# Optimization experiments

Hardware: AMD Instinct MI355X
Metric: run time of the kernel (lower is better)

## Reference

```python
import jax, jax.numpy as jnp
import numpy as np

N_NODES = 50000
N_EDGES = 800000
HIDDEN = 128
N_GRAPHS = 64


def _linear_init(key, fan_in, shape):
    # torch.nn.Linear default init: U(-1/sqrt(fan_in), 1/sqrt(fan_in))
    bound = 1.0 / np.sqrt(fan_in)
    return jax.random.uniform(key, shape, jnp.float32, -bound, bound)


def setup_inputs() -> dict:
    key = jax.random.key(0)
    ks = jax.random.split(key, 13)
    x = jax.random.normal(ks[0], (N_NODES, HIDDEN), jnp.float32)
    edge_index = jax.random.randint(ks[1], (2, N_EDGES), 0, N_NODES, dtype=jnp.int64)
    batch = jnp.sort(jax.random.randint(ks[2], (N_NODES,), 0, N_GRAPHS, dtype=jnp.int64))
    H = HIDDEN
    return {
        "x": x,
        "edge_index": edge_index,
        "batch": batch,
        "W1a": _linear_init(ks[3], H, (H, H)),
        "b1a": _linear_init(ks[4], H, (H,)),
        "W2a": _linear_init(ks[5], H, (H, H)),
        "b2a": _linear_init(ks[6], H, (H,)),
        "W1b": _linear_init(ks[7], H, (H, H)),
        "b1b": _linear_init(ks[8], H, (H,)),
        "W2b": _linear_init(ks[9], H, (H, H)),
        "b2b": _linear_init(ks[10], H, (H,)),
        "Wfc": _linear_init(ks[11], H, (H, 1)),
        "bfc": _linear_init(ks[12], H, (1,)),
    }


def _gin_conv(x, src, dst, W1, b1, W2, b2):
    # GINConv with eps=0: mlp((1+eps)*x + sum_{j->i} x_j)
    agg = jax.ops.segment_sum(x[src], dst, num_segments=N_NODES) + x
    h = jax.nn.gelu(agg @ W1 + b1, approximate=False)  # exact erf GELU (torch default)
    return jax.nn.gelu(h @ W2 + b2, approximate=False)


def reference(x, edge_index, batch, W1a, b1a, W2a, b2a, W1b, b1b, W2b, b2b, Wfc, bfc):
    src, dst = edge_index[0], edge_index[1]  # messages flow src -> dst (PyG convention)
    h = _gin_conv(x, src, dst, W1a, b1a, W2a, b2a)
    h = _gin_conv(h, src, dst, W1b, b1b, W2b, b2b)
    y = h @ Wfc + bfc  # [N, 1]
    return jax.ops.segment_sum(y, batch, num_segments=N_GRAPHS)  # [G, 1]
```

## Files before the change

kernel.cpp:

```cpp
#include <hip/hip_runtime.h>
#include <hip/hip_bf16.h>
#include <math.h>

#define N_NODES 50000
#define N_EDGES 800000
#define HID 128
#define N_GRAPHS 64
#define BCAP 64

typedef __bf16 bfv8 __attribute__((ext_vector_type(8)));
typedef float f32x4 __attribute__((ext_vector_type(4)));

__device__ __forceinline__ unsigned short f2bf(float f) {
    unsigned int u = __float_as_uint(f);
    u += 0x7fff + ((u >> 16) & 1);
    return (unsigned short)(u >> 16);
}
__device__ __forceinline__ float bflo(unsigned int u) { return __uint_as_float(u << 16); }
__device__ __forceinline__ float bfhi(unsigned int u) { return __uint_as_float(u & 0xffff0000u); }

__device__ __forceinline__ float gelu_f(float x) {
    float x3 = x * x * x;
    float z = 1.5957691216f * x + 0.0713548162f * x3;
    float e = __expf(z);
    float t = 1.f - 2.f / (e + 1.f);
    return 0.5f * x * (1.f + t);
}

__global__ void conv_bf16(const float4* __restrict__ in, ushort4* __restrict__ out, int n4) {
    for (int i = blockIdx.x * blockDim.x + threadIdx.x; i < n4; i += gridDim.x * blockDim.x) {
        float4 v = in[i];
        ushort4 o;
        o.x = f2bf(v.x); o.y = f2bf(v.y); o.z = f2bf(v.z); o.w = f2bf(v.w);
        out[i] = o;
    }
}

__global__ void prep_weights(const float* __restrict__ W1a, const float* __restrict__ W2a,
                             const float* __restrict__ W1b, const float* __restrict__ W2b,
                             unsigned short* __restrict__ out) {
    int i = blockIdx.x * blockDim.x + threadIdx.x;
    if (i >= 4 * HID * HID) return;
    int m = i >> 14;
    int r = (i >> 7) & 127;
    int c = i & 127;
    const float* W = (m == 0) ? W1a : (m == 1) ? W2a : (m == 2) ? W1b : W2b;
    out[i] = f2bf(W[c * HID + r]);
}

__global__ void bucket_insert(const int* __restrict__ src, const int* __restrict__ dst,
                              int* __restrict__ counts, unsigned short* __restrict__ bucket) {
    int e = blockIdx.x * blockDim.x + threadIdx.x;
    if (e < N_EDGES) {
        int d = dst[e];
        int pos = atomicAdd(&counts[d], 1);
        if (pos < BCAP) bucket[(size_t)d * BCAP + pos] = (unsigned short)src[e];
    }
}

__global__ __launch_bounds__(256) void aggregate8(const unsigned short* __restrict__ xb,
                                                  const int* __restrict__ counts,
                                                  const unsigned short* __restrict__ bucket,
                                                  unsigned short* __restrict__ agg) {
    int node = blockIdx.x * 4 + (threadIdx.x >> 6);
    if (node >= N_NODES) return;
    int lane = threadIdx.x & 63;
    int g = lane >> 3;
    int c = lane & 7;
    int cnt = min(counts[node], BCAP);
    int eidx = (int)bucket[(size_t)node * BCAP + lane];
    float a[16];
    #pragma unroll
    for (int j = 0; j < 16; ++j) a[j] = 0.f;
    int kmax = (cnt + 7) >> 3;
    #pragma unroll 2
    for (int k = 0; k < kmax; ++k) {
        int i = 8 * k + g;
        int s = __shfl(eidx, (i < cnt) ? i : 0);
        if (i < cnt) {
            const unsigned short* row = xb + (size_t)s * HID + c * 16;
            uint4 u0 = *(const uint4*)(row);
            uint4 u1 = *(const uint4*)(row + 8);
            a[0] += bflo(u0.x); a[1] += bfhi(u0.x);
            a[2] += bflo(u0.y); a[3] += bfhi(u0.y);
            a[4] += bflo(u0.z); a[5] += bfhi(u0.z);
            a[6] += bflo(u0.w); a[7] += bfhi(u0.w);
            a[8] += bflo(u1.x); a[9] += bfhi(u1.x);
            a[10] += bflo(u1.y); a[11] += bfhi(u1.y);
            a[12] += bflo(u1.z); a[13] += bfhi(u1.z);
            a[14] += bflo(u1.w); a[15] += bfhi(u1.w);
        }
    }
    #pragma unroll
    for (int j = 0; j < 16; ++j) {
        a[j] += __shfl_xor(a[j], 8);
        a[j] += __shfl_xor(a[j], 16);
        a[j] += __shfl_xor(a[j], 32);
    }
    if (g == 0) {
        const unsigned short* row = xb + (size_t)node * HID + c * 16;
        uint4 u0 = *(const uint4*)(row);
        uint4 u1 = *(const uint4*)(row + 8);
        a[0] += bflo(u0.x); a[1] += bfhi(u0.x);
        a[2] += bflo(u0.y); a[3] += bfhi(u0.y);
        a[4] += bflo(u0.z); a[5] += bfhi(u0.z);
        a[6] += bflo(u0.w); a[7] += bfhi(u0.w);
        a[8] += bflo(u1.x); a[9] += bfhi(u1.x);
        a[10] += bflo(u1.y); a[11] += bfhi(u1.y);
        a[12] += bflo(u1.z); a[13] += bfhi(u1.z);
        a[14] += bflo(u1.w); a[15] += bfhi(u1.w);
        uint4 o0, o1;
        o0.x = (unsigned int)f2bf(a[0]) | ((unsigned int)f2bf(a[1]) << 16);
        o0.y = (unsigned int)f2bf(a[2]) | ((unsigned int)f2bf(a[3]) << 16);
        o0.z = (unsigned int)f2bf(a[4]) | ((unsigned int)f2bf(a[5]) << 16);
        o0.w = (unsigned int)f2bf(a[6]) | ((unsigned int)f2bf(a[7]) << 16);
        o1.x = (unsigned int)f2bf(a[8]) | ((unsigned int)f2bf(a[9]) << 16);
        o1.y = (unsigned int)f2bf(a[10]) | ((unsigned int)f2bf(a[11]) << 16);
        o1.z = (unsigned int)f2bf(a[12]) | ((unsigned int)f2bf(a[13]) << 16);
        o1.w = (unsigned int)f2bf(a[14]) | ((unsigned int)f2bf(a[15]) << 16);
        unsigned short* orow = agg + (size_t)node * HID + c * 16;
        *(uint4*)(orow) = o0;
        *(uint4*)(orow + 8) = o1;
    }
}

#define LDP 136
__global__ __launch_bounds__(512) void mlp_fused(const unsigned short* __restrict__ A,
                                                 const unsigned short* __restrict__ Wt1,
                                                 const float* __restrict__ b1,
                                                 const unsigned short* __restrict__ Wt2,
                                                 const float* __restrict__ b2,
                                                 unsigned short* __restrict__ out, int nrows) {
    __shared__ __align__(16) unsigned short sA[128][LDP];
    __shared__ __align__(16) unsigned short sT[128][LDP];
    const int t = threadIdx.x;
    const int row0 = blockIdx.x * 128;

    #pragma unroll
    for (int rr = 0; rr < 4; ++rr) {
        int idx = t + rr * 512;
        int r = idx >> 4;
        int cb = (idx & 15) * 8;
        int gr = row0 + r;
        ulonglong2 v = {0ull, 0ull};
        if (gr < nrows) v = *(const ulonglong2*)(A + (size_t)gr * HID + cb);
        *(ulonglong2*)(&sA[r][cb]) = v;
    }

    const int w = t >> 6;
    const int l = t & 63;
    const int lr = l & 15;
    const int lkg = l >> 4;
    const int lk = lkg * 8;
    const int cw = w * 16 + lr;

    bfv8 w1f[4], w2f[4];
    #pragma unroll
    for (int kc = 0; kc < 4; ++kc) {
        w1f[kc] = *(const bfv8*)(Wt1 + (size_t)cw * HID + kc * 32 + lk);
        w2f[kc] = *(const bfv8*)(Wt2 + (size_t)cw * HID + kc * 32 + lk);
    }
    float bias1 = b1[cw];
    float bias2 = b2[cw];
    __syncthreads();

    f32x4 acc[8];
    #pragma unroll
    for (int m = 0; m < 8; ++m) acc[m] = (f32x4){0.f, 0.f, 0.f, 0.f};
    #pragma unroll
    for (int m = 0; m < 8; ++m) {
        #pragma unroll
        for (int kc = 0; kc < 4; ++kc) {
            bfv8 af = *(const bfv8*)(&sA[m * 16 + lr][kc * 32 + lk]);
            acc[m] = __builtin_amdgcn_mfma_f32_16x16x32_bf16(af, w1f[kc], acc[m], 0, 0, 0);
        }
    }
    #pragma unroll
    for (int m = 0; m < 8; ++m) {
        #pragma unroll
        for (int i = 0; i < 4; ++i) {
            float v = gelu_f(acc[m][i] + bias1);
            sT[m * 16 + lkg * 4 + i][cw] = f2bf(v);
        }
    }
    __syncthreads();

    #pragma unroll
    for (int m = 0; m < 8; ++m) acc[m] = (f32x4){0.f, 0.f, 0.f, 0.f};
    #pragma unroll
    for (int m = 0; m < 8; ++m) {
        #pragma unroll
        for (int kc = 0; kc < 4; ++kc) {
            bfv8 af = *(const bfv8*)(&sT[m * 16 + lr][kc * 32 + lk]);
            acc[m] = __builtin_amdgcn_mfma_f32_16x16x32_bf16(af, w2f[kc], acc[m], 0, 0, 0);
        }
    }
    #pragma unroll
    for (int m = 0; m < 8; ++m) {
        #pragma unroll
        for (int i = 0; i < 4; ++i) {
            float v = gelu_f(acc[m][i] + bias2);
            sA[m * 16 + lkg * 4 + i][cw] = f2bf(v);
        }
    }
    __syncthreads();
    #pragma unroll
    for (int rr = 0; rr < 4; ++rr) {
        int idx = t + rr * 512;
        int r = idx >> 4;
        int cb = (idx & 15) * 8;
        int gr = row0 + r;
        if (gr < nrows)
            *(ulonglong2*)(out + (size_t)gr * HID + cb) = *(const ulonglong2*)(&sA[r][cb]);
    }
}

__global__ __launch_bounds__(512) void mlp_final(const unsigned short* __restrict__ A,
                                                 const unsigned short* __restrict__ Wt1,
                                                 const float* __restrict__ b1,
                                                 const unsigned short* __restrict__ Wt2,
                                                 const float* __restrict__ b2,
                                                 const float* __restrict__ Wfc,
                                                 const float* __restrict__ bfc,
                                                 const int* __restrict__ batch,
                                                 float* __restrict__ out, int nrows) {
    __shared__ __align__(16) unsigned short sA[128][LDP];
    __shared__ __align__(16) unsigned short sT[128][LDP];
    __shared__ float bins[N_GRAPHS];
    const int t = threadIdx.x;
    const int row0 = blockIdx.x * 128;
    if (t < N_GRAPHS) bins[t] = 0.f;

    #pragma unroll
    for (int rr = 0; rr < 4; ++rr) {
        int idx = t + rr * 512;
        int r = idx >> 4;
        int cb = (idx & 15) * 8;
        int gr = row0 + r;
        ulonglong2 v = {0ull, 0ull};
        if (gr < nrows) v = *(const ulonglong2*)(A + (size_t)gr * HID + cb);
        *(ulonglong2*)(&sA[r][cb]) = v;
    }

    const int w = t >> 6;
    const int l = t & 63;
    const int lr = l & 15;
    const int lkg = l >> 4;
    const int lk = lkg * 8;
    const int cw = w * 16 + lr;

    bfv8 w1f[4], w2f[4];
    #pragma unroll
    for (int kc = 0; kc < 4; ++kc) {
        w1f[kc] = *(const bfv8*)(Wt1 + (size_t)cw * HID + kc * 32 + lk);
        w2f[kc] = *(const bfv8*)(Wt2 + (size_t)cw * HID + kc * 32 + lk);
    }
    float bias1 = b1[cw];
    float bias2 = b2[cw];
    __syncthreads();

    f32x4 acc[8];
    #pragma unroll
    for (int m = 0; m < 8; ++m) acc[m] = (f32x4){0.f, 0.f, 0.f, 0.f};
    #pragma unroll
    for (int m = 0; m < 8; ++m) {
        #pragma unroll
        for (int kc = 0; kc < 4; ++kc) {
            bfv8 af = *(const bfv8*)(&sA[m * 16 + lr][kc * 32 + lk]);
            acc[m] = __builtin_amdgcn_mfma_f32_16x16x32_bf16(af, w1f[kc], acc[m], 0, 0, 0);
        }
    }
    #pragma unroll
    for (int m = 0; m < 8; ++m) {
        #pragma unroll
        for (int i = 0; i < 4; ++i) {
            float v = gelu_f(acc[m][i] + bias1);
            sT[m * 16 + lkg * 4 + i][cw] = f2bf(v);
        }
    }
    __syncthreads();

    #pragma unroll
    for (int m = 0; m < 8; ++m) acc[m] = (f32x4){0.f, 0.f, 0.f, 0.f};
    #pragma unroll
    for (int m = 0; m < 8; ++m) {
        #pragma unroll
        for (int kc = 0; kc < 4; ++kc) {
            bfv8 af = *(const bfv8*)(&sT[m * 16 + lr][kc * 32 + lk]);
            acc[m] = __builtin_amdgcn_mfma_f32_16x16x32_bf16(af, w2f[kc], acc[m], 0, 0, 0);
        }
    }
    #pragma unroll
    for (int m = 0; m < 8; ++m) {
        #pragma unroll
        for (int i = 0; i < 4; ++i) {
            float v = gelu_f(acc[m][i] + bias2);
            sA[m * 16 + lkg * 4 + i][cw] = f2bf(v);
        }
    }
    __syncthreads();

    {
        int row = w * 16 + (l >> 2);
        int q = l & 3;
        int gr = row0 + row;
        float acc2 = 0.f;
        if (gr < nrows) {
            const uint4* hrow = (const uint4*)(&sA[row][q * 32]);
            #pragma unroll
            for (int jj = 0; jj < 4; ++jj) {
                uint4 v = hrow[jj];
                int f = q * 32 + jj * 8;
                acc2 += bflo(v.x) * Wfc[f]     + bfhi(v.x) * Wfc[f + 1];
                acc2 += bflo(v.y) * Wfc[f + 2] + bfhi(v.y) * Wfc[f + 3];
                acc2 += bflo(v.z) * Wfc[f + 4] + bfhi(v.z) * Wfc[f + 5];
                acc2 += bflo(v.w) * Wfc[f + 6] + bfhi(v.w) * Wfc[f + 7];
            }
        }
        acc2 += __shfl_xor(acc2, 1);
        acc2 += __shfl_xor(acc2, 2);
        if (q == 0 && gr < nrows) atomicAdd(&bins[batch[gr]], acc2 + bfc[0]);
    }
    __syncthreads();
    if (t < N_GRAPHS && bins[t] != 0.f) atomicAdd(&out[t], bins[t]);
}

extern "C" void kernel_launch(void* const* d_in, const int* in_sizes, int n_in,
                              void* d_out, int out_size, void* d_ws, size_t ws_size,
                              hipStream_t stream) {
    const float* x    = (const float*)d_in[0];
    const int*   ei   = (const int*)d_in[1];
    const int*   bat  = (const int*)d_in[2];
    const float* W1a  = (const float*)d_in[3];
    const float* b1a  = (const float*)d_in[4];
    const float* W2a  = (const float*)d_in[5];
    const float* b2a  = (const float*)d_in[6];
    const float* W1b  = (const float*)d_in[7];
    const float* b1b  = (const float*)d_in[8];
    const float* W2b  = (const float*)d_in[9];
    const float* b2b  = (const float*)d_in[10];
    const float* Wfc  = (const float*)d_in[11];
    const float* bfc  = (const float*)d_in[12];
    float* out = (float*)d_out;

    const int* src = ei;
    const int* dst = ei + N_EDGES;

    unsigned short* xb     = (unsigned short*)d_ws;
    unsigned short* bufA   = xb + (size_t)N_NODES * HID;
    unsigned short* bufB   = bufA + (size_t)N_NODES * HID;
    unsigned short* Wt     = bufB + (size_t)N_NODES * HID;
    int* counts = (int*)(Wt + 4 * HID * HID);
    unsigned short* bucket = (unsigned short*)(counts + N_NODES);

    hipMemsetAsync(out, 0, N_GRAPHS * sizeof(float), stream);
    hipMemsetAsync(counts, 0, N_NODES * sizeof(int), stream);

    conv_bf16<<<1024, 256, 0, stream>>>((const float4*)x, (ushort4*)xb, N_NODES * HID / 4);
    prep_weights<<<(4 * HID * HID + 255) / 256, 256, 0, stream>>>(W1a, W2a, W1b, W2b, Wt);

    bucket_insert<<<(N_EDGES + 255) / 256, 256, 0, stream>>>(src, dst, counts, bucket);

    const int agg_blocks = (N_NODES + 3) / 4;
    const int mlp_blocks = (N_NODES + 127) / 128;
    unsigned short* Wt1a = Wt;
    unsigned short* Wt2a = Wt + HID * HID;
    unsigned short* Wt1b = Wt + 2 * HID * HID;
    unsigned short* Wt2b = Wt + 3 * HID * HID;

    aggregate8<<<agg_blocks, 256, 0, stream>>>(xb, counts, bucket, bufA);
    mlp_fused<<<mlp_blocks, 512, 0, stream>>>(bufA, Wt1a, b1a, Wt2a, b2a, bufB, N_NODES);

    aggregate8<<<agg_blocks, 256, 0, stream>>>(bufB, counts, bucket, bufA);
    mlp_final<<<mlp_blocks, 512, 0, stream>>>(bufA, Wt1b, b1b, Wt2b, b2b,
                                              Wfc, bfc, bat, out, N_NODES);
}
```

Baseline: 258.4 us.

## Fuse bf16 conversion, weight prep and range-partitioned bucket insert into one kernel

Merges the x-to-bf16 conversion, the weight transpose/convert and the edge bucketing into a single launch whose blocks each take one role, removing two kernel launches and letting the three independent jobs overlap. Bucket insertion now has each edge chunk read by four blocks, and each block inserts only the edges whose destination falls in its quarter of the node range. This is meant to localise the atomics and bucket writes, at the cost of reading dst four times. Bucket order within a node changes but the sums stay the same up to float ordering.

```diff
diff --git a/kernel.cpp b/kernel.cpp
--- a/kernel.cpp
+++ b/kernel.cpp
@@ -7,6 +7,14 @@
 #define HID 128
 #define N_GRAPHS 64
 #define BCAP 64
+
+#define ELOOP 8
+#define EB ((N_EDGES + 256 * ELOOP - 1) / (256 * ELOOP))
+#define RANGES 4
+#define RSPAN ((N_NODES + RANGES - 1) / RANGES)
+#define CONV_B 782
+#define PREP_B 256
+#define PREP_GRID (EB * RANGES + CONV_B + PREP_B)
 
 typedef __bf16 bfv8 __attribute__((ext_vector_type(8)));
 typedef float f32x4 __attribute__((ext_vector_type(4)));
@@ -27,34 +35,52 @@
     return 0.5f * x * (1.f + t);
 }
 
-__global__ void conv_bf16(const float4* __restrict__ in, ushort4* __restrict__ out, int n4) {
-    for (int i = blockIdx.x * blockDim.x + threadIdx.x; i < n4; i += gridDim.x * blockDim.x) {
-        float4 v = in[i];
-        ushort4 o;
-        o.x = f2bf(v.x); o.y = f2bf(v.y); o.z = f2bf(v.z); o.w = f2bf(v.w);
-        out[i] = o;
-    }
-}
-
-__global__ void prep_weights(const float* __restrict__ W1a, const float* __restrict__ W2a,
-                             const float* __restrict__ W1b, const float* __restrict__ W2b,
-                             unsigned short* __restrict__ out) {
-    int i = blockIdx.x * blockDim.x + threadIdx.x;
-    if (i >= 4 * HID * HID) return;
-    int m = i >> 14;
-    int r = (i >> 7) & 127;
-    int c = i & 127;
-    const float* W = (m == 0) ? W1a : (m == 1) ? W2a : (m == 2) ? W1b : W2b;
-    out[i] = f2bf(W[c * HID + r]);
-}
-
-__global__ void bucket_insert(const int* __restrict__ src, const int* __restrict__ dst,
-                              int* __restrict__ counts, unsigned short* __restrict__ bucket) {
-    int e = blockIdx.x * blockDim.x + threadIdx.x;
-    if (e < N_EDGES) {
-        int d = dst[e];
-        int pos = atomicAdd(&counts[d], 1);
-        if (pos < BCAP) bucket[(size_t)d * BCAP + pos] = (unsigned short)src[e];
+__global__ __launch_bounds__(256) void prep_all(
+    const int* __restrict__ src, const int* __restrict__ dst,
+    int* __restrict__ counts, unsigned short* __restrict__ bucket,
+    const float4* __restrict__ xin, ushort4* __restrict__ xb4,
+    const float* __restrict__ W1a, const float* __restrict__ W2a,
+    const float* __restrict__ W1b, const float* __restrict__ W2b,
+    unsigned short* __restrict__ Wt) {
+    int b = blockIdx.x;
+    int t = threadIdx.x;
+    if (b < EB * RANGES) {
+        int r = b % RANGES;
+        int chunk = b / RANGES;
+        int lo = r * RSPAN;
+        int hi = min(lo + RSPAN, N_NODES);
+        int e0 = chunk * (256 * ELOOP) + t;
+        #pragma unroll
+        for (int j = 0; j < ELOOP; ++j) {
+            int e = e0 + j * 256;
+            if (e < N_EDGES) {
+                int d = dst[e];
+                if (d >= lo && d < hi) {
+                    int pos = atomicAdd(&counts[d], 1);
+                    if (pos < BCAP) bucket[(size_t)d * BCAP + pos] = (unsigned short)src[e];
+                }
+            }
+        }
+    } else if (b < EB * RANGES + CONV_B) {
+        int bc = b - EB * RANGES;
+        const int n4 = N_NODES * HID / 4;
+        #pragma unroll
+        for (int j = 0; j < 8; ++j) {
+            int i = bc * 2048 + j * 256 + t;
+            if (i < n4) {
+                float4 v = xin[i];
+                ushort4 o;
+                o.x = f2bf(v.x); o.y = f2bf(v.y); o.z = f2bf(v.z); o.w = f2bf(v.w);
+                xb4[i] = o;
+            }
+        }
+    } else {
+        int i = (b - EB * RANGES - CONV_B) * 256 + t;
+        int m = i >> 14;
+        int rr = (i >> 7) & 127;
+        int cc = i & 127;
+        const float* W = (m == 0) ? W1a : (m == 1) ? W2a : (m == 2) ? W1b : W2b;
+        Wt[i] = f2bf(W[cc * HID + rr]);
     }
 }
 
@@ -356,10 +382,9 @@
     hipMemsetAsync(out, 0, N_GRAPHS * sizeof(float), stream);
     hipMemsetAsync(counts, 0, N_NODES * sizeof(int), stream);
 
-    conv_bf16<<<1024, 256, 0, stream>>>((const float4*)x, (ushort4*)xb, N_NODES * HID / 4);
-    prep_weights<<<(4 * HID * HID + 255) / 256, 256, 0, stream>>>(W1a, W2a, W1b, W2b, Wt);
-
-    bucket_insert<<<(N_EDGES + 255) / 256, 256, 0, stream>>>(src, dst, counts, bucket);
+    prep_all<<<PREP_GRID, 256, 0, stream>>>(src, dst, counts, bucket,
+                                            (const float4*)x, (ushort4*)xb,
+                                            W1a, W2a, W1b, W2b, Wt);
 
     const int agg_blocks = (N_NODES + 3) / 4;
     const int mlp_blocks = (N_NODES + 127) / 128;
```

Measured after the change: 238.6 us. 7.7% less time.
